# Performance work log

Hardware: AMD Instinct MI355X
Metric: run time of the kernel (lower is better)

Reference implementation:

```python
import jax, jax.numpy as jnp
import numpy as np


def setup_inputs() -> dict:
    key = jax.random.key(0)
    k1, k2 = jax.random.split(key)
    B, C, M, N = 4, 3, 4096, 8192
    query = jax.random.normal(k1, (B, C, M), dtype=jnp.float32)
    points = jax.random.normal(k2, (B, C, N), dtype=jnp.float32)
    return {"k": 16, "query": query, "points": points}


def reference(k, query, points):
    # query: BxCxM, points: BxCxN  (trans=True path of original module)
    q = jnp.swapaxes(query, 1, 2)   # BxMxC
    p = jnp.swapaxes(points, 1, 2)  # BxNxC
    # squared L2 distances (FAISS GpuIndexFlatL2): BxMxN
    q2 = jnp.sum(q * q, axis=-1, keepdims=True)           # BxMx1
    p2 = jnp.sum(p * p, axis=-1)[:, None, :]              # Bx1xN
    dist = q2 + p2 - 2.0 * jnp.einsum('bmc,bnc->bmn', q, p)
    # k smallest distances, sorted ascending (FAISS sorts results)
    _, index_batch = jax.lax.top_k(-dist, k)              # BxMxK int32
    index_batch = index_batch.astype(jnp.int64) if index_batch.dtype != jnp.int64 else index_batch
    # gather neighbor coordinates: points BxCxN, idx BxMxK -> BxCxMxK
    neighbor_points = jax.vmap(lambda pts, idx: pts[:, idx])(points, index_batch)
    return neighbor_points, index_batch
```

## Files before the change

kernel.cpp:

```cpp
#include <hip/hip_runtime.h>
#include <stdint.h>

#define BQ 4
#define CC 3
#define MM 4096
#define NN 8192
#define KK 16
#define NP_OFF (BQ*CC*MM*KK)
#define BLOCK 256
#define WAVES 4
#define RPW 4
#define ROWS (WAVES*RPW)
#define CHUNK 1024
#define NCH (NN/CHUNK)
#define CST (CHUNK/64)
#define EPSD 1e-4f

__device__ __forceinline__ float rfl(float x) {
    return __uint_as_float((unsigned)__builtin_amdgcn_readfirstlane((int)__float_as_uint(x)));
}

__global__ __launch_bounds__(BLOCK, 4) void knn_kernel(
    const float* __restrict__ query,
    const float* __restrict__ points,
    float* __restrict__ out)
{
    __shared__ float4 pts[2][CHUNK];
    __shared__ unsigned cand[ROWS][64];
    __shared__ unsigned scnt[ROWS];

    const int tid  = threadIdx.x;
    const int lane = tid & 63;
    const int wv   = tid >> 6;
    const int bid  = blockIdx.x;
    const int b    = bid >> 8;
    const int rb   = (bid & 255) * ROWS;

    const float* pb = points + b * (CC * NN);
    const float* qb = query  + b * (CC * MM);

    if (tid < ROWS) scnt[tid] = 0;

    float qx[RPW], qy[RPW], qz[RPW], q2[RPW], dm[RPW];
    #pragma unroll
    for (int r = 0; r < RPW; ++r) {
        int m = rb + wv * RPW + r;
        float x = rfl(qb[m]);
        float y = rfl(qb[MM + m]);
        float z = rfl(qb[2*MM + m]);
        qx[r] = x; qy[r] = y; qz[r] = z;
        q2[r] = rfl(__fadd_rn(__fadd_rn(__fmul_rn(x,x), __fmul_rn(y,y)),
                              __fmul_rn(z,z)));
        dm[r] = -__builtin_inff();
    }

    auto stage = [&](int ch, int bi) {
        #pragma unroll
        for (int i = 0; i < CHUNK / BLOCK; ++i) {
            int ii = i * BLOCK + tid;
            int n  = ch * CHUNK + ii;
            float px = pb[n], py = pb[NN + n], pz = pb[2*NN + n];
            float p2 = __fadd_rn(__fadd_rn(__fmul_rn(px,px), __fmul_rn(py,py)),
                                 __fmul_rn(pz,pz));
            pts[bi][ii] = make_float4(px, py, pz, -0.5f * p2);
        }
    };

    auto comp1 = [&](int bi) {
        #pragma unroll
        for (int t = 0; t < CST; ++t) {
            float4 P = pts[bi][(t << 6) + lane];
            #pragma unroll
            for (int r = 0; r < RPW; ++r) {
                float dotf = __builtin_fmaf(qz[r], P.z,
                              __builtin_fmaf(qy[r], P.y,
                               __builtin_fmaf(qx[r], P.x, P.w)));
                dm[r] = fmaxf(dm[r], dotf);
            }
        }
    };

    stage(0, 0);
    #pragma unroll 1
    for (int ch = 0; ch < NCH; ch += 2) {
        __syncthreads();
        if (ch + 1 < NCH) stage(ch + 1, 1);
        comp1(0);
        __syncthreads();
        if (ch + 2 < NCH) stage(ch + 2, 0);
        if (ch + 1 < NCH) comp1(1);
    }

    float rc[RPW];
    #pragma unroll
    for (int r = 0; r < RPW; ++r) {
        float v = dm[r];
        #pragma unroll
        for (int k = 2; k <= 64; k <<= 1) {
            #pragma unroll
            for (int j = k >> 1; j > 0; j >>= 1) {
                float o = __shfl_xor(v, j, 64);
                bool keepmin = (((lane & j) == 0) == ((lane & k) == 0));
                v = keepmin ? fminf(v, o) : fmaxf(v, o);
            }
        }
        float tau = __shfl(v, 64 - KK, 64);
        rc[r] = rfl(tau - EPSD);
    }

    auto comp2 = [&](int ch, int bi) {
        #pragma unroll
        for (int t = 0; t < CST; ++t) {
            float4 P = pts[bi][(t << 6) + lane];
            unsigned n = (unsigned)(ch * CHUNK + (t << 6) + lane);
            #pragma unroll
            for (int r = 0; r < RPW; ++r) {
                float dotf = __builtin_fmaf(qz[r], P.z,
                              __builtin_fmaf(qy[r], P.y,
                               __builtin_fmaf(qx[r], P.x, P.w)));
                if (dotf >= rc[r]) {
                    unsigned pos = atomicAdd(&scnt[wv*RPW + r], 1u);
                    if (pos < 64u) cand[wv*RPW + r][pos] = n;
                }
            }
        }
    };

    stage(0, 0);
    #pragma unroll 1
    for (int ch = 0; ch < NCH; ch += 2) {
        __syncthreads();
        if (ch + 1 < NCH) stage(ch + 1, 1);
        comp2(ch, 0);
        __syncthreads();
        if (ch + 2 < NCH) stage(ch + 2, 0);
        if (ch + 1 < NCH) comp2(ch + 1, 1);
    }
    __syncthreads();

    #pragma unroll
    for (int r = 0; r < RPW; ++r) {
        int row = wv * RPW + r;
        unsigned c = scnt[row]; if (c > 64u) c = 64u;
        unsigned kb = 0xffffffffu, id = 0xffffffffu;
        if (lane < (int)c) {
            id = cand[row][lane];
            float px = pb[id], py = pb[NN + id], pz = pb[2*NN + id];
            float p2 = __fadd_rn(__fadd_rn(__fmul_rn(px,px), __fmul_rn(py,py)),
                                 __fmul_rn(pz,pz));
            float dot = __builtin_fmaf(qz[r], pz,
                         __builtin_fmaf(qy[r], py, __fmul_rn(qx[r], px)));
            float d = __fsub_rn(__fadd_rn(q2[r], p2), __fmul_rn(2.0f, dot));
            unsigned fb = __float_as_uint(d);
            kb = (fb & 0x80000000u) ? ~fb : (fb | 0x80000000u);
        }
        #pragma unroll
        for (int k = 2; k <= 64; k <<= 1) {
            #pragma unroll
            for (int j = k >> 1; j > 0; j >>= 1) {
                unsigned ok = __shfl_xor(kb, j, 64);
                unsigned oi = __shfl_xor(id, j, 64);
                bool takeMin  = (((lane & j) == 0) == ((lane & k) == 0));
                bool selfLess = (kb < ok) || (kb == ok && id < oi);
                if (selfLess != takeMin) { kb = ok; id = oi; }
            }
        }
        if (lane < KK) {
            int m  = rb + row;
            int oi = (int)id;
            out[NP_OFF + (b * MM + m) * KK + lane] = (float)oi;
            out[((b * CC + 0) * MM + m) * KK + lane] = pb[oi];
            out[((b * CC + 1) * MM + m) * KK + lane] = pb[NN + oi];
            out[((b * CC + 2) * MM + m) * KK + lane] = pb[2*NN + oi];
        }
    }
}

extern "C" void kernel_launch(void* const* d_in, const int* in_sizes, int n_in,
                              void* d_out, int out_size, void* d_ws, size_t ws_size,
                              hipStream_t stream) {
    const float* query  = (const float*)d_in[1];
    const float* points = (const float*)d_in[2];
    float* out = (float*)d_out;
    dim3 grid(BQ * (MM / ROWS));
    dim3 block(BLOCK);
    knn_kernel<<<grid, block, 0, stream>>>(query, points, out);
}
```

Before: 113.8 us.

## Split each query row group across two waves covering halves of point chunks

```diff
diff --git a/kernel.cpp b/kernel.cpp
--- a/kernel.cpp
+++ b/kernel.cpp
@@ -7,20 +7,21 @@
 #define NN 8192
 #define KK 16
 #define NP_OFF (BQ*CC*MM*KK)
-#define BLOCK 256
-#define WAVES 4
+#define BLOCK 512
 #define RPW 4
-#define ROWS (WAVES*RPW)
+#define GROUPS 4
+#define ROWS (GROUPS*RPW)
 #define CHUNK 1024
 #define NCH (NN/CHUNK)
 #define CST (CHUNK/64)
+#define HST (CST/2)
 #define EPSD 1e-4f
 
 __device__ __forceinline__ float rfl(float x) {
     return __uint_as_float((unsigned)__builtin_amdgcn_readfirstlane((int)__float_as_uint(x)));
 }
 
-__global__ __launch_bounds__(BLOCK, 4) void knn_kernel(
+__global__ __launch_bounds__(BLOCK, 8) void knn_kernel(
     const float* __restrict__ query,
     const float* __restrict__ points,
     float* __restrict__ out)
@@ -28,10 +29,13 @@
     __shared__ float4 pts[2][CHUNK];
     __shared__ unsigned cand[ROWS][64];
     __shared__ unsigned scnt[ROWS];
+    __shared__ float taub[ROWS][32];
 
     const int tid  = threadIdx.x;
     const int lane = tid & 63;
     const int wv   = tid >> 6;
+    const int g    = wv >> 1;
+    const int h    = wv & 1;
     const int bid  = blockIdx.x;
     const int b    = bid >> 8;
     const int rb   = (bid & 255) * ROWS;
@@ -44,7 +48,7 @@
     float qx[RPW], qy[RPW], qz[RPW], q2[RPW], dm[RPW];
     #pragma unroll
     for (int r = 0; r < RPW; ++r) {
-        int m = rb + wv * RPW + r;
+        int m = rb + g * RPW + r;
         float x = rfl(qb[m]);
         float y = rfl(qb[MM + m]);
         float z = rfl(qb[2*MM + m]);
@@ -68,8 +72,8 @@
 
     auto comp1 = [&](int bi) {
         #pragma unroll
-        for (int t = 0; t < CST; ++t) {
-            float4 P = pts[bi][(t << 6) + lane];
+        for (int t = 0; t < HST; ++t) {
+            float4 P = pts[bi][((h * HST + t) << 6) + lane];
             #pragma unroll
             for (int r = 0; r < RPW; ++r) {
                 float dotf = __builtin_fmaf(qz[r], P.z,
@@ -91,7 +95,6 @@
         if (ch + 1 < NCH) comp1(1);
     }
 
-    float rc[RPW];
     #pragma unroll
     for (int r = 0; r < RPW; ++r) {
         float v = dm[r];
@@ -104,23 +107,40 @@
                 v = keepmin ? fminf(v, o) : fmaxf(v, o);
             }
         }
-        float tau = __shfl(v, 64 - KK, 64);
+        if (lane >= 48) taub[g*RPW + r][h*16 + lane - 48] = v;
+    }
+    __syncthreads();
+    float rc[RPW];
+    #pragma unroll
+    for (int r = 0; r < RPW; ++r) {
+        float v = (lane < 32) ? taub[g*RPW + r][lane] : -__builtin_inff();
+        #pragma unroll
+        for (int k = 2; k <= 64; k <<= 1) {
+            #pragma unroll
+            for (int j = k >> 1; j > 0; j >>= 1) {
+                float o = __shfl_xor(v, j, 64);
+                bool keepmin = (((lane & j) == 0) == ((lane & k) == 0));
+                v = keepmin ? fminf(v, o) : fmaxf(v, o);
+            }
+        }
+        float tau = __shfl(v, 48, 64);
         rc[r] = rfl(tau - EPSD);
     }
 
     auto comp2 = [&](int ch, int bi) {
         #pragma unroll
-        for (int t = 0; t < CST; ++t) {
-            float4 P = pts[bi][(t << 6) + lane];
-            unsigned n = (unsigned)(ch * CHUNK + (t << 6) + lane);
+        for (int t = 0; t < HST; ++t) {
+            int st = h * HST + t;
+            float4 P = pts[bi][(st << 6) + lane];
+            unsigned n = (unsigned)(ch * CHUNK + (st << 6) + lane);
             #pragma unroll
             for (int r = 0; r < RPW; ++r) {
                 float dotf = __builtin_fmaf(qz[r], P.z,
                               __builtin_fmaf(qy[r], P.y,
                                __builtin_fmaf(qx[r], P.x, P.w)));
                 if (dotf >= rc[r]) {
-                    unsigned pos = atomicAdd(&scnt[wv*RPW + r], 1u);
-                    if (pos < 64u) cand[wv*RPW + r][pos] = n;
+                    unsigned pos = atomicAdd(&scnt[g*RPW + r], 1u);
+                    if (pos < 64u) cand[g*RPW + r][pos] = n;
                 }
             }
         }
@@ -139,8 +159,9 @@
     __syncthreads();
 
     #pragma unroll
-    for (int r = 0; r < RPW; ++r) {
-        int row = wv * RPW + r;
+    for (int rr = 0; rr < 2; ++rr) {
+        int r   = 2*h + rr;
+        int row = g * RPW + r;
         unsigned c = scnt[row]; if (c > 64u) c = 64u;
         unsigned kb = 0xffffffffu, id = 0xffffffffu;
         if (lane < (int)c) {
```

New measurement: 115.7 us. Within noise of the previous version (+1.7%).
